# Performance work log

Measured on AMD Instinct MI355X. Metric: run time of the kernel, lower is better.

## Reference

```python
import jax, jax.numpy as jnp
import numpy as np

D_MODEL = 1024
NUM_HEADS = 16
HEAD_DIM = D_MODEL // NUM_HEADS


def setup_inputs() -> dict:
    key = jax.random.key(0)
    ks = jax.random.split(key, 10)
    B, SQ, SKV = 4, 2048, 2048
    s = 1.0 / np.sqrt(D_MODEL)
    return {
        "query": jax.random.normal(ks[0], (B, SQ, D_MODEL), jnp.float32),
        "key_value": jax.random.normal(ks[1], (B, SKV, D_MODEL), jnp.float32),
        "Wq": jax.random.normal(ks[2], (D_MODEL, D_MODEL), jnp.float32) * s,
        "bq": jnp.zeros((D_MODEL,), jnp.float32),
        "Wk": jax.random.normal(ks[3], (D_MODEL, D_MODEL), jnp.float32) * s,
        "bk": jnp.zeros((D_MODEL,), jnp.float32),
        "Wv": jax.random.normal(ks[4], (D_MODEL, D_MODEL), jnp.float32) * s,
        "bv": jnp.zeros((D_MODEL,), jnp.float32),
        "Wo": jax.random.normal(ks[5], (D_MODEL, D_MODEL), jnp.float32) * s,
        "bo": jnp.zeros((D_MODEL,), jnp.float32),
    }


def reference(query, key_value, Wq, bq, Wk, bk, Wv, bv, Wo, bo):
    B, SQ, _ = query.shape
    SKV = key_value.shape[1]
    H, Dh = NUM_HEADS, HEAD_DIM
    # projections (torch Linear: x @ W.T + b); split heads -> (B, H, S, Dh)
    Q = (query @ Wq.T + bq).reshape(B, SQ, H, Dh).transpose(0, 2, 1, 3)
    K = (key_value @ Wk.T + bk).reshape(B, SKV, H, Dh).transpose(0, 2, 1, 3)
    V = (key_value @ Wv.T + bv).reshape(B, SKV, H, Dh).transpose(0, 2, 1, 3)
    scale = jnp.asarray(np.sqrt(Dh), query.dtype)
    scores = jnp.einsum("bhqd,bhkd->bhqk", Q, K) / scale
    weights = jax.nn.softmax(scores, axis=-1)  # dropout is identity in eval
    attn = jnp.einsum("bhqk,bhkd->bhqd", weights, V)
    attn = attn.transpose(0, 2, 1, 3).reshape(B, SQ, H * Dh)
    return attn @ Wo.T + bo
```

## Files before the change

### kernel.cpp

```cpp
#include <hip/hip_runtime.h>

#define NH 16
#define DH 64
#define DM 1024
#define SEQ 2048
#define BATCH 4
#define NT 16

typedef short s16x8 __attribute__((ext_vector_type(8)));
typedef float f32x4 __attribute__((ext_vector_type(4)));

__device__ __forceinline__ unsigned short f2bf(float f) {
  union { float f; unsigned int u; } v; v.f = f;
  unsigned int u = v.u;
  unsigned int r = (u + 0x7fffu + ((u >> 16) & 1u)) >> 16;
  return (unsigned short)r;
}

__device__ __forceinline__ unsigned int pkbf(float a, float b) {
#if __has_builtin(__builtin_amdgcn_cvt_pk_bf16_f32)
  typedef short v2s __attribute__((ext_vector_type(2)));
  v2s r = __builtin_amdgcn_cvt_pk_bf16_f32(a, b);
  union { v2s v; unsigned int u; } cv; cv.v = r;
  return cv.u;
#else
  return (unsigned int)f2bf(a) | ((unsigned int)f2bf(b) << 16);
#endif
}

__device__ __forceinline__ float fexp2(float x) {
#if __has_builtin(__builtin_amdgcn_exp2f)
  return __builtin_amdgcn_exp2f(x);
#else
  return exp2f(x);
#endif
}

__device__ __forceinline__ void gload_lds16(const void* g, void* l) {
  __builtin_amdgcn_global_load_lds(
      (const __attribute__((address_space(1))) unsigned int*)g,
      (__attribute__((address_space(3))) unsigned int*)l, 16, 0, 0);
}

#define GBAR() asm volatile("s_barrier" ::: "memory")

__global__ void convert_all(const float* __restrict__ q, const float* __restrict__ kv,
                            const float* __restrict__ w0, const float* __restrict__ w1,
                            const float* __restrict__ w2, const float* __restrict__ w3,
                            unsigned short* __restrict__ oq, unsigned short* __restrict__ okv,
                            unsigned short* __restrict__ ow0, unsigned short* __restrict__ ow1,
                            unsigned short* __restrict__ ow2, unsigned short* __restrict__ ow3) {
  const int NQ4 = (BATCH * SEQ * DM) / 4;
  const int NW4 = (DM * DM) / 4;
  const int total = NQ4 * 2 + NW4 * 4;
  for (int i = blockIdx.x * blockDim.x + threadIdx.x; i < total;
       i += gridDim.x * blockDim.x) {
    const float* s; unsigned short* d; int off;
    if (i < NQ4)            { s = q;  d = oq;  off = i; }
    else if (i < 2 * NQ4)   { s = kv; d = okv; off = i - NQ4; }
    else {
      int j = i - 2 * NQ4; int wsel = j / NW4; off = j - wsel * NW4;
      s = (wsel == 0) ? w0 : (wsel == 1) ? w1 : (wsel == 2) ? w2 : w3;
      d = (wsel == 0) ? ow0 : (wsel == 1) ? ow1 : (wsel == 2) ? ow2 : ow3;
    }
    float4 v = *(const float4*)(s + (size_t)off * 4);
    ushort4 o;
    o.x = f2bf(v.x); o.y = f2bf(v.y); o.z = f2bf(v.z); o.w = f2bf(v.w);
    *(ushort4*)(d + (size_t)off * 4) = o;
  }
}

template <int NJ>
__device__ __forceinline__ void stage_rows(const unsigned short* __restrict__ src,
                                           int row0, int kt,
                                           unsigned short* __restrict__ dst, int tid) {
  const int sr = tid >> 3;
  const int g8 = ((tid & 7) ^ (sr & 7)) * 8;
  const int wv = tid >> 6;
#pragma unroll
  for (int j = 0; j < NJ; ++j)
    gload_lds16(src + (size_t)(row0 + j * 64 + sr) * DM + kt + g8,
                dst + (j * 8 + wv) * 512);
}

__device__ __forceinline__ void gemm256_tile(const unsigned short* __restrict__ X,
                                             const unsigned short* __restrict__ Wt,
                                             unsigned short* __restrict__ SM,
                                             int m0, int n0, f32x4 (*acc)[4]) {
  const int tid = threadIdx.x;
  const int wv = tid >> 6, lane = tid & 63;
  const int quad = lane >> 4, c = lane & 15;
  const int wr = wv >> 2, wc = wv & 3;
  unsigned short* A0 = SM;
  unsigned short* B0 = SM + 8192;
  unsigned short* A1 = SM + 24576;
  unsigned short* B1 = SM + 24576 + 8192;

  stage_rows<2>(X, m0, 0, A0, tid);
  stage_rows<4>(Wt, n0, 0, B0, tid);
  stage_rows<2>(X, m0, 64, A1, tid);
  stage_rows<4>(Wt, n0, 64, B1, tid);
  asm volatile("s_waitcnt vmcnt(6)" ::: "memory");
  GBAR();

  const int rA0 = wr * 64 + c;
  const int rB0 = wc * 64 + c;
  const int c7 = c & 7;

  for (int t = 0; t < NT; ++t) {
    unsigned short* A_ = (t & 1) ? A1 : A0;
    unsigned short* B_ = (t & 1) ? B1 : B0;
    unsigned short* An = (t & 1) ? A0 : A1;

    s16x8 af[2][2], bf[4][2];
#pragma unroll
    for (int fm = 0; fm < 2; ++fm)
#pragma unroll
      for (int k2 = 0; k2 < 2; ++k2)
        af[fm][k2] = *(const s16x8*)(A_ + (rA0 + fm * 16) * 64 +
                                     (((k2 * 4 + quad) ^ c7) * 8));
#pragma unroll
    for (int fn = 0; fn < 4; ++fn)
#pragma unroll
      for (int k2 = 0; k2 < 2; ++k2)
        bf[fn][k2] = *(const s16x8*)(B_ + (rB0 + fn * 16) * 64 +
                                     (((k2 * 4 + quad) ^ c7) * 8));
    if (t >= 1 && t + 1 < NT)
      stage_rows<2>(X, m0, (t + 1) * 64, An, tid);
    GBAR();
    __builtin_amdgcn_s_setprio(1);
#pragma unroll
    for (int k2 = 0; k2 < 2; ++k2)
#pragma unroll
      for (int fm = 0; fm < 2; ++fm)
#pragma unroll
        for (int fn = 0; fn < 4; ++fn)
          acc[fm][fn] = __builtin_amdgcn_mfma_f32_16x16x32_bf16(
              af[fm][k2], bf[fn][k2], acc[fm][fn], 0, 0, 0);
    __builtin_amdgcn_s_setprio(0);
    GBAR();

#pragma unroll
    for (int fm = 0; fm < 2; ++fm)
#pragma unroll
      for (int k2 = 0; k2 < 2; ++k2)
        af[fm][k2] = *(const s16x8*)(A_ + (rA0 + (fm + 2) * 16) * 64 +
                                     (((k2 * 4 + quad) ^ c7) * 8));
    if (t + 2 < NT) {
      stage_rows<4>(Wt, n0, (t + 2) * 64, B_, tid);
      asm volatile("s_waitcnt vmcnt(4)" ::: "memory");
    } else {
      asm volatile("s_waitcnt vmcnt(0)" ::: "memory");
    }
    GBAR();
    __builtin_amdgcn_s_setprio(1);
#pragma unroll
    for (int k2 = 0; k2 < 2; ++k2)
#pragma unroll
      for (int fm = 0; fm < 2; ++fm)
#pragma unroll
        for (int fn = 0; fn < 4; ++fn)
          acc[fm + 2][fn] = __builtin_amdgcn_mfma_f32_16x16x32_bf16(
              af[fm][k2], bf[fn][k2], acc[fm + 2][fn], 0, 0, 0);
    __builtin_amdgcn_s_setprio(0);
    GBAR();
  }
}

__global__ __launch_bounds__(512, 2)
void gemm_qkv256(const unsigned short* __restrict__ Xq,
                 const unsigned short* __restrict__ Xkv,
                 const unsigned short* __restrict__ W0,
                 const unsigned short* __restrict__ W1,
                 const unsigned short* __restrict__ W2,
                 const float* __restrict__ b0, const float* __restrict__ b1,
                 const float* __restrict__ b2,
                 unsigned short* __restrict__ OQ, unsigned short* __restrict__ OK_,
                 unsigned short* __restrict__ OV) {
  __shared__ alignas(16) unsigned short SM[49152];
  const int m0 = blockIdx.x * 128;
  const int ysel = blockIdx.y >> 2;
  const int n0 = (blockIdx.y & 3) * 256;
  const unsigned short* X = (ysel == 0) ? Xq : Xkv;
  const unsigned short* Wt = (ysel == 0) ? W0 : (ysel == 1) ? W1 : W2;
  const float* bias = (ysel == 0) ? b0 : (ysel == 1) ? b1 : b2;
  unsigned short* Out = (ysel == 0) ? OQ : (ysel == 1) ? OK_ : OV;
  const float scale = (ysel == 0) ? 0.1803368801f : 1.0f;

  f32x4 acc[4][4] = {};
  gemm256_tile(X, Wt, SM, m0, n0, acc);

  const int tid = threadIdx.x;
  const int wv = tid >> 6, lane = tid & 63;
  const int quad = lane >> 4, c = lane & 15;
  const int wr = wv >> 2, wc = wv & 3;
  const int m0w = m0 + wr * 64;
  const int n0w = n0 + wc * 64;
#pragma unroll
  for (int fm = 0; fm < 4; ++fm) {
#pragma unroll
    for (int fn = 0; fn < 4; ++fn) {
      int n = n0w + fn * 16 + c;
      float bv = bias[n];
      int m_base = m0w + fm * 16 + quad * 4;
      if (ysel == 2) {
        int b_ = m_base >> 11, s_ = m_base & 2047, h_ = n >> 6, dh = n & 63;
        size_t idx = (((size_t)(b_ * NH + h_)) * DH + dh) * SEQ + s_;
        ushort4 o4;
        o4.x = f2bf(acc[fm][fn][0] + bv);
        o4.y = f2bf(acc[fm][fn][1] + bv);
        o4.z = f2bf(acc[fm][fn][2] + bv);
        o4.w = f2bf(acc[fm][fn][3] + bv);
        *(ushort4*)(&Out[idx]) = o4;
      } else {
#pragma unroll
        for (int p = 0; p < 4; ++p) {
          int m = m_base + p;
          float val = (acc[fm][fn][p] + bv) * scale;
          int b_ = m >> 11, s_ = m & 2047, h_ = n >> 6, dh = n & 63;
          size_t idx = (((size_t)(b_ * NH + h_)) * SEQ + s_) * DH + dh;
          Out[idx] = f2bf(val);
        }
      }
    }
  }
}

__global__ __launch_bounds__(512, 2)
void gemm_o256(const unsigned short* __restrict__ X,
               const unsigned short* __restrict__ Wt,
               const float* __restrict__ bias, float* __restrict__ Out) {
  __shared__ alignas(16) unsigned short SM[49152];
  const int m0 = blockIdx.x * 128;
  const int n0 = blockIdx.y * 256;
  f32x4 acc[4][4] = {};
  gemm256_tile(X, Wt, SM, m0, n0, acc);

  const int tid = threadIdx.x;
  const int wv = tid >> 6, lane = tid & 63;
  const int quad = lane >> 4, c = lane & 15;
  const int wr = wv >> 2, wc = wv & 3;
  const int m0w = m0 + wr * 64;
  const int n0w = n0 + wc * 64;
#pragma unroll
  for (int fm = 0; fm < 4; ++fm) {
#pragma unroll
    for (int fn = 0; fn < 4; ++fn) {
      int n = n0w + fn * 16 + c;
      float bv = bias[n];
#pragma unroll
      for (int p = 0; p < 4; ++p) {
        int m = m0w + fm * 16 + quad * 4 + p;
        Out[(size_t)m * DM + n] = acc[fm][fn][p] + bv;
      }
    }
  }
}

__global__ __launch_bounds__(256, 4)
void attn_kernel(const unsigned short* __restrict__ Qb,
                 const unsigned short* __restrict__ Kb,
                 const unsigned short* __restrict__ VTb,
                 unsigned short* __restrict__ Ob) {
  __shared__ alignas(16) unsigned short SM[16384];

  const int tid = threadIdx.x, wv_ = tid >> 6, lane = tid & 63;
  const int quad = lane >> 4, c = lane & 15;
  const int bh = blockIdx.x, qb = blockIdx.y;
  const unsigned short* Qp = Qb + (size_t)bh * SEQ * DH;
  const unsigned short* Kp = Kb + (size_t)bh * SEQ * DH;
  const unsigned short* Vp = VTb + (size_t)bh * DH * SEQ;
  const int wq0 = qb * 128 + wv_ * 32;

  s16x8 aq[2][2];
#pragma unroll
  for (int t = 0; t < 2; ++t)
#pragma unroll
    for (int k2 = 0; k2 < 2; ++k2)
      aq[t][k2] = *(const s16x8*)(Qp + (size_t)(wq0 + t * 16 + c) * DH +
                                  k2 * 32 + quad * 8);

  f32x4 ot[4][2] = {};
  float lsum[2] = {};

  const int srow = lane >> 3;
  const int schunk = (lane & 7) ^ srow;

#pragma unroll
  for (int i = 0; i < 2; ++i) {
    int reg = wv_ * 2 + i;
    gload_lds16(Kp + (size_t)(reg * 8 + srow) * DH + schunk * 8,
                (void*)(SM + reg * 512));
    gload_lds16(Vp + (size_t)(reg * 8 + srow) * SEQ + schunk * 8,
                (void*)(SM + 8192 + reg * 512));
  }

  for (int kt = 0; kt < SEQ; kt += 64) {
    const int cur = (kt >> 6) & 1;
    __syncthreads();
    if (kt + 64 < SEQ) {
      const int nxt = cur ^ 1;
#pragma unroll
      for (int i = 0; i < 2; ++i) {
        int reg = wv_ * 2 + i;
        gload_lds16(Kp + (size_t)(kt + 64 + reg * 8 + srow) * DH + schunk * 8,
                    (void*)(SM + nxt * 4096 + reg * 512));
        gload_lds16(Vp + (size_t)(reg * 8 + srow) * SEQ + kt + 64 + schunk * 8,
                    (void*)(SM + 8192 + nxt * 4096 + reg * 512));
      }
    }
    const unsigned short* K_ = SM + cur * 4096;
    const unsigned short* V_ = SM + 8192 + cur * 4096;

    f32x4 s[2][2][2] = {};
#pragma unroll
    for (int k2 = 0; k2 < 2; ++k2) {
      s16x8 ak[2][2];
#pragma unroll
      for (int jp = 0; jp < 2; ++jp)
#pragma unroll
        for (int h = 0; h < 2; ++h) {
          int r = jp * 32 + ((c >> 2) << 3) + h * 4 + (c & 3);
          int g = k2 * 4 + quad;
          ak[jp][h] = *(const s16x8*)(K_ + r * 64 + ((g ^ (r & 7)) * 8));
        }
#pragma unroll
      for (int t = 0; t < 2; ++t)
#pragma unroll
        for (int jp = 0; jp < 2; ++jp)
#pragma unroll
          for (int h = 0; h < 2; ++h)
            s[t][jp][h] = __builtin_amdgcn_mfma_f32_16x16x32_bf16(
                ak[jp][h], aq[t][k2], s[t][jp][h], 0, 0, 0);
    }

    s16x8 bp[2][2];
#pragma unroll
    for (int t = 0; t < 2; ++t)
#pragma unroll
      for (int jp = 0; jp < 2; ++jp) {
        float e00 = fexp2(s[t][jp][0][0]);
        float e01 = fexp2(s[t][jp][0][1]);
        float e02 = fexp2(s[t][jp][0][2]);
        float e03 = fexp2(s[t][jp][0][3]);
        float e10 = fexp2(s[t][jp][1][0]);
        float e11 = fexp2(s[t][jp][1][1]);
        float e12 = fexp2(s[t][jp][1][2]);
        float e13 = fexp2(s[t][jp][1][3]);
        lsum[t] += ((e00 + e01) + (e02 + e03)) + ((e10 + e11) + (e12 + e13));
        union { s16x8 v; unsigned int u[4]; } pk;
        pk.u[0] = pkbf(e00, e01);
        pk.u[1] = pkbf(e02, e03);
        pk.u[2] = pkbf(e10, e11);
        pk.u[3] = pkbf(e12, e13);
        bp[t][jp] = pk.v;
      }

#pragma unroll
    for (int jp = 0; jp < 2; ++jp)
#pragma unroll
      for (int dt = 0; dt < 4; ++dt) {
        int g = jp * 4 + quad;
        int r = dt * 16 + c;
        s16x8 av = *(const s16x8*)(V_ + r * 64 + ((g ^ (r & 7)) * 8));
#pragma unroll
        for (int t = 0; t < 2; ++t)
          ot[dt][t] = __builtin_amdgcn_mfma_f32_16x16x32_bf16(
              av, bp[t][jp], ot[dt][t], 0, 0, 0);
      }
  }

#pragma unroll
  for (int t = 0; t < 2; ++t) {
    lsum[t] += __shfl_xor(lsum[t], 16);
    lsum[t] += __shfl_xor(lsum[t], 32);
  }

  __syncthreads();

  unsigned short* Lq = SM + wv_ * (32 * 72);
#pragma unroll
  for (int t = 0; t < 2; ++t) {
    float inv = 1.0f / lsum[t];
#pragma unroll
    for (int dt = 0; dt < 4; ++dt) {
      unsigned int w01 = pkbf(ot[dt][t][0] * inv, ot[dt][t][1] * inv);
      unsigned int w23 = pkbf(ot[dt][t][2] * inv, ot[dt][t][3] * inv);
      unsigned short* p = Lq + (t * 16 + c) * 72 + dt * 16 + quad * 4;
      *(unsigned int*)(p) = w01;
      *(unsigned int*)(p + 2) = w23;
    }
  }
  const int b_ = bh >> 4, h_ = bh & 15;
  const int ql = lane >> 1, hf = lane & 1;
  const unsigned short* Lr = Lq + ql * 72 + hf * 32;
  unsigned short* Og = Ob + ((size_t)(b_ * SEQ + wq0 + ql)) * DM + h_ * 64 + hf * 32;
#pragma unroll
  for (int j = 0; j < 4; ++j) {
    s16x8 v = *(const s16x8*)(Lr + j * 8);
    *(s16x8*)(Og + j * 8) = v;
  }
}

extern "C" void kernel_launch(void* const* d_in, const int* in_sizes, int n_in,
                              void* d_out, int out_size, void* d_ws, size_t ws_size,
                              hipStream_t stream) {
  const float* q  = (const float*)d_in[0];
  const float* kv = (const float*)d_in[1];
  const float* Wq = (const float*)d_in[2];
  const float* bq = (const float*)d_in[3];
  const float* Wk = (const float*)d_in[4];
  const float* bk = (const float*)d_in[5];
  const float* Wv = (const float*)d_in[6];
  const float* bv = (const float*)d_in[7];
  const float* Wo = (const float*)d_in[8];
  const float* bo = (const float*)d_in[9];

  char* ws = (char*)d_ws;
  const size_t MB = 1024 * 1024;
  unsigned short* q_bf  = (unsigned short*)(ws);
  unsigned short* kv_bf = (unsigned short*)(ws + 16 * MB);
  unsigned short* wq_bf = (unsigned short*)(ws + 32 * MB);
  unsigned short* wk_bf = (unsigned short*)(ws + 34 * MB);
  unsigned short* wv_bf = (unsigned short*)(ws + 36 * MB);
  unsigned short* wo_bf = (unsigned short*)(ws + 38 * MB);
  unsigned short* Qb    = (unsigned short*)(ws + 40 * MB);
  unsigned short* Kb    = (unsigned short*)(ws + 56 * MB);
  unsigned short* VTb   = (unsigned short*)(ws + 72 * MB);
  unsigned short* attn  = (unsigned short*)(ws + 88 * MB);

  convert_all<<<2048, 256, 0, stream>>>(q, kv, Wq, Wk, Wv, Wo,
                                        q_bf, kv_bf, wq_bf, wk_bf, wv_bf, wo_bf);
  gemm_qkv256<<<dim3(64, 12), 512, 0, stream>>>(q_bf, kv_bf, wq_bf, wk_bf, wv_bf,
                                                bq, bk, bv, Qb, Kb, VTb);
  attn_kernel<<<dim3(64, 16), 256, 0, stream>>>(Qb, Kb, VTb, attn);
  gemm_o256<<<dim3(64, 4), 512, 0, stream>>>(attn, wo_bf, bo, (float*)d_out);
}
```

Baseline: 328.3 us.

## Enlarge projection GEMM tiles to 256x256 with 8-phase pipeline and block swizzle

Replaces the 128x256 GEMM tile with a 256x256 tile in both projection GEMMs. Each wave now computes 128x64 with 32 accumulators, and the K loop becomes an eight-phase schedule that interleaves half-slab global-to-LDS loads with LDS reads and MFMA bursts. Workgroup indices are swizzled so neighbouring blocks share operand rows. The aim is more reuse per loaded byte and better L2 locality, at the cost of 128KB LDS, more registers and only 384/128 blocks, which may underfill the CUs.

```diff
diff --git a/kernel.cpp b/kernel.cpp
--- a/kernel.cpp
+++ b/kernel.cpp
@@ -43,6 +43,7 @@
 }
 
 #define GBAR() asm volatile("s_barrier" ::: "memory")
+#define LG0()  asm volatile("s_waitcnt lgkmcnt(0)" ::: "memory")
 
 __global__ void convert_all(const float* __restrict__ q, const float* __restrict__ kv,
                             const float* __restrict__ w0, const float* __restrict__ w1,
@@ -70,134 +71,163 @@
   }
 }
 
-template <int NJ>
-__device__ __forceinline__ void stage_rows(const unsigned short* __restrict__ src,
+__device__ __forceinline__ void stage_slab(const unsigned short* __restrict__ src,
                                            int row0, int kt,
-                                           unsigned short* __restrict__ dst, int tid) {
+                                           unsigned short* __restrict__ lds, int tid) {
   const int sr = tid >> 3;
   const int g8 = ((tid & 7) ^ (sr & 7)) * 8;
-  const int wv = tid >> 6;
-#pragma unroll
-  for (int j = 0; j < NJ; ++j)
-    gload_lds16(src + (size_t)(row0 + j * 64 + sr) * DM + kt + g8,
-                dst + (j * 8 + wv) * 512);
-}
-
-__device__ __forceinline__ void gemm256_tile(const unsigned short* __restrict__ X,
-                                             const unsigned short* __restrict__ Wt,
-                                             unsigned short* __restrict__ SM,
-                                             int m0, int n0, f32x4 (*acc)[4]) {
+  gload_lds16(src + (size_t)(row0 + sr) * DM + kt + g8,
+              lds + (tid >> 6) * 512);
+}
+
+__device__ __forceinline__ void rd4(const unsigned short* __restrict__ base,
+                                    int xg, s16x8 (&f)[4]) {
+#pragma unroll
+  for (int j = 0; j < 4; ++j)
+    f[j] = *(const s16x8*)(base + j * 1024 + xg);
+}
+
+template <int H>
+__device__ __forceinline__ void mm16(s16x8 (&af)[4], s16x8 (&bf)[4],
+                                     f32x4 (*acc)[4]) {
+  __builtin_amdgcn_s_setprio(1);
+#pragma unroll
+  for (int j = 0; j < 4; ++j)
+#pragma unroll
+    for (int fn = 0; fn < 4; ++fn)
+      acc[H * 4 + j][fn] = __builtin_amdgcn_mfma_f32_16x16x32_bf16(
+          af[j], bf[fn], acc[H * 4 + j][fn], 0, 0, 0);
+  __builtin_amdgcn_s_setprio(0);
+}
+
+__device__ __forceinline__ void gemm8p_tile(const unsigned short* __restrict__ X,
+                                            const unsigned short* __restrict__ Wt,
+                                            unsigned short* __restrict__ SM,
+                                            int m0, int n0, f32x4 (*acc)[4]) {
   const int tid = threadIdx.x;
   const int wv = tid >> 6, lane = tid & 63;
   const int quad = lane >> 4, c = lane & 15;
   const int wr = wv >> 2, wc = wv & 3;
-  unsigned short* A0 = SM;
-  unsigned short* B0 = SM + 8192;
-  unsigned short* A1 = SM + 24576;
-  unsigned short* B1 = SM + 24576 + 8192;
-
-  stage_rows<2>(X, m0, 0, A0, tid);
-  stage_rows<4>(Wt, n0, 0, B0, tid);
-  stage_rows<2>(X, m0, 64, A1, tid);
-  stage_rows<4>(Wt, n0, 64, B1, tid);
-  asm volatile("s_waitcnt vmcnt(6)" ::: "memory");
+  const int rA = (wr * 128 + c) * 64;
+  const int rB = (wc * 64 + c) * 64;
+  const int xg0 = (quad ^ (c & 7)) * 8;
+  const int xg1 = ((4 + quad) ^ (c & 7)) * 8;
+  const int A0 = 0, B0 = 16384, A1 = 32768, B1 = 49152;
+
+  s16x8 af[4], bf[4];
+
+  stage_slab(Wt, n0,       0, SM + B0,         tid);
+  stage_slab(Wt, n0 + 64,  0, SM + B0 + 4096,  tid);
+  stage_slab(Wt, n0 + 128, 0, SM + B0 + 8192,  tid);
+  stage_slab(Wt, n0 + 192, 0, SM + B0 + 12288, tid);
+  stage_slab(X,  m0,       0, SM + A0,         tid);
+  stage_slab(X,  m0 + 128, 0, SM + A0 + 8192,  tid);
+  stage_slab(X,  m0 + 64,  0, SM + A0 + 4096,  tid);
+  stage_slab(X,  m0 + 192, 0, SM + A0 + 12288, tid);
+  stage_slab(Wt, n0,       64, SM + B1,        tid);
+  stage_slab(Wt, n0 + 64,  64, SM + B1 + 4096, tid);
+  stage_slab(X,  m0,       64, SM + A1,        tid);
+  stage_slab(X,  m0 + 128, 64, SM + A1 + 8192, tid);
+  asm volatile("s_waitcnt vmcnt(4)" ::: "memory");
   GBAR();
 
-  const int rA0 = wr * 64 + c;
-  const int rB0 = wc * 64 + c;
-  const int c7 = c & 7;
-
-  for (int t = 0; t < NT; ++t) {
-    unsigned short* A_ = (t & 1) ? A1 : A0;
-    unsigned short* B_ = (t & 1) ? B1 : B0;
-    unsigned short* An = (t & 1) ? A0 : A1;
-
-    s16x8 af[2][2], bf[4][2];
-#pragma unroll
-    for (int fm = 0; fm < 2; ++fm)
-#pragma unroll
-      for (int k2 = 0; k2 < 2; ++k2)
-        af[fm][k2] = *(const s16x8*)(A_ + (rA0 + fm * 16) * 64 +
-                                     (((k2 * 4 + quad) ^ c7) * 8));
-#pragma unroll
-    for (int fn = 0; fn < 4; ++fn)
-#pragma unroll
-      for (int k2 = 0; k2 < 2; ++k2)
-        bf[fn][k2] = *(const s16x8*)(B_ + (rB0 + fn * 16) * 64 +
-                                     (((k2 * 4 + quad) ^ c7) * 8));
-    if (t >= 1 && t + 1 < NT)
-      stage_rows<2>(X, m0, (t + 1) * 64, An, tid);
-    GBAR();
-    __builtin_amdgcn_s_setprio(1);
-#pragma unroll
-    for (int k2 = 0; k2 < 2; ++k2)
-#pragma unroll
-      for (int fm = 0; fm < 2; ++fm)
-#pragma unroll
-        for (int fn = 0; fn < 4; ++fn)
-          acc[fm][fn] = __builtin_amdgcn_mfma_f32_16x16x32_bf16(
-              af[fm][k2], bf[fn][k2], acc[fm][fn], 0, 0, 0);
-    __builtin_amdgcn_s_setprio(0);
-    GBAR();
-
-#pragma unroll
-    for (int fm = 0; fm < 2; ++fm)
-#pragma unroll
-      for (int k2 = 0; k2 < 2; ++k2)
-        af[fm][k2] = *(const s16x8*)(A_ + (rA0 + (fm + 2) * 16) * 64 +
-                                     (((k2 * 4 + quad) ^ c7) * 8));
-    if (t + 2 < NT) {
-      stage_rows<4>(Wt, n0, (t + 2) * 64, B_, tid);
+  for (int i = 0; i < NT / 2; ++i) {
+    const int t1k = (2 * i + 1) * 64;
+    const int t2 = 2 * i + 2, t3 = 2 * i + 3;
+    const int t2k = t2 * 64, t3k = t3 * 64;
+
+    rd4(SM + B0 + rB, xg0, bf);
+    rd4(SM + A0 + rA, xg0, af);
+    stage_slab(Wt, n0 + 128, t1k, SM + B1 + 8192,  tid);
+    stage_slab(Wt, n0 + 192, t1k, SM + B1 + 12288, tid);
+    stage_slab(X,  m0 + 64,  t1k, SM + A1 + 4096,  tid);
+    stage_slab(X,  m0 + 192, t1k, SM + A1 + 12288, tid);
+    GBAR(); LG0(); mm16<0>(af, bf, acc); GBAR();
+
+    rd4(SM + A0 + rA + 4096, xg0, af);
+    GBAR(); LG0(); mm16<1>(af, bf, acc); GBAR();
+
+    rd4(SM + B0 + rB, xg1, bf);
+    rd4(SM + A0 + rA, xg1, af);
+    GBAR(); LG0(); mm16<0>(af, bf, acc); GBAR();
+
+    rd4(SM + A0 + rA + 4096, xg1, af);
+    if (t2 < NT) {
+      stage_slab(Wt, n0,       t2k, SM + B0,        tid);
+      stage_slab(Wt, n0 + 64,  t2k, SM + B0 + 4096, tid);
+      stage_slab(X,  m0,       t2k, SM + A0,        tid);
+      stage_slab(X,  m0 + 128, t2k, SM + A0 + 8192, tid);
       asm volatile("s_waitcnt vmcnt(4)" ::: "memory");
     } else {
       asm volatile("s_waitcnt vmcnt(0)" ::: "memory");
     }
-    GBAR();
-    __builtin_amdgcn_s_setprio(1);
-#pragma unroll
-    for (int k2 = 0; k2 < 2; ++k2)
-#pragma unroll
-      for (int fm = 0; fm < 2; ++fm)
-#pragma unroll
-        for (int fn = 0; fn < 4; ++fn)
-          acc[fm + 2][fn] = __builtin_amdgcn_mfma_f32_16x16x32_bf16(
-              af[fm][k2], bf[fn][k2], acc[fm + 2][fn], 0, 0, 0);
-    __builtin_amdgcn_s_setprio(0);
-    GBAR();
+    GBAR(); LG0(); mm16<1>(af, bf, acc); GBAR();
+
+    rd4(SM + B1 + rB, xg0, bf);
+    rd4(SM + A1 + rA, xg0, af);
+    if (t2 < NT) {
+      stage_slab(Wt, n0 + 128, t2k, SM + B0 + 8192,  tid);
+      stage_slab(Wt, n0 + 192, t2k, SM + B0 + 12288, tid);
+      stage_slab(X,  m0 + 64,  t2k, SM + A0 + 4096,  tid);
+      stage_slab(X,  m0 + 192, t2k, SM + A0 + 12288, tid);
+    }
+    GBAR(); LG0(); mm16<0>(af, bf, acc); GBAR();
+
+    rd4(SM + A1 + rA + 4096, xg0, af);
+    GBAR(); LG0(); mm16<1>(af, bf, acc); GBAR();
+
+    rd4(SM + B1 + rB, xg1, bf);
+    rd4(SM + A1 + rA, xg1, af);
+    GBAR(); LG0(); mm16<0>(af, bf, acc); GBAR();
+
+    rd4(SM + A1 + rA + 4096, xg1, af);
+    if (t3 < NT) {
+      stage_slab(Wt, n0,       t3k, SM + B1,        tid);
+      stage_slab(Wt, n0 + 64,  t3k, SM + B1 + 4096, tid);
+      stage_slab(X,  m0,       t3k, SM + A1,        tid);
+      stage_slab(X,  m0 + 128, t3k, SM + A1 + 8192, tid);
+      asm volatile("s_waitcnt vmcnt(4)" ::: "memory");
+    } else {
+      asm volatile("s_waitcnt vmcnt(0)" ::: "memory");
+    }
+    GBAR(); LG0(); mm16<1>(af, bf, acc); GBAR();
   }
 }
 
 __global__ __launch_bounds__(512, 2)
-void gemm_qkv256(const unsigned short* __restrict__ Xq,
-                 const unsigned short* __restrict__ Xkv,
-                 const unsigned short* __restrict__ W0,
-                 const unsigned short* __restrict__ W1,
-                 const unsigned short* __restrict__ W2,
-                 const float* __restrict__ b0, const float* __restrict__ b1,
-                 const float* __restrict__ b2,
-                 unsigned short* __restrict__ OQ, unsigned short* __restrict__ OK_,
-                 unsigned short* __restrict__ OV) {
-  __shared__ alignas(16) unsigned short SM[49152];
-  const int m0 = blockIdx.x * 128;
-  const int ysel = blockIdx.y >> 2;
-  const int n0 = (blockIdx.y & 3) * 256;
+void gemm_qkv8p(const unsigned short* __restrict__ Xq,
+                const unsigned short* __restrict__ Xkv,
+                const unsigned short* __restrict__ W0,
+                const unsigned short* __restrict__ W1,
+                const unsigned short* __restrict__ W2,
+                const float* __restrict__ b0, const float* __restrict__ b1,
+                const float* __restrict__ b2,
+                unsigned short* __restrict__ OQ, unsigned short* __restrict__ OK_,
+                unsigned short* __restrict__ OV) {
+  __shared__ alignas(16) unsigned short SM[65536];
+  const int wg = blockIdx.y * 32 + blockIdx.x;
+  const int swz = (wg & 7) * 48 + (wg >> 3);
+  const int m0 = (swz & 31) * 256;
+  const int yy = swz >> 5;
+  const int ysel = yy >> 2;
+  const int n0 = (yy & 3) * 256;
   const unsigned short* X = (ysel == 0) ? Xq : Xkv;
   const unsigned short* Wt = (ysel == 0) ? W0 : (ysel == 1) ? W1 : W2;
   const float* bias = (ysel == 0) ? b0 : (ysel == 1) ? b1 : b2;
   unsigned short* Out = (ysel == 0) ? OQ : (ysel == 1) ? OK_ : OV;
   const float scale = (ysel == 0) ? 0.1803368801f : 1.0f;
 
-  f32x4 acc[4][4] = {};
-  gemm256_tile(X, Wt, SM, m0, n0, acc);
+  f32x4 acc[8][4] = {};
+  gemm8p_tile(X, Wt, SM, m0, n0, acc);
 
   const int tid = threadIdx.x;
   const int wv = tid >> 6, lane = tid & 63;
   const int quad = lane >> 4, c = lane & 15;
   const int wr = wv >> 2, wc = wv & 3;
-  const int m0w = m0 + wr * 64;
+  const int m0w = m0 + wr * 128;
   const int n0w = n0 + wc * 64;
 #pragma unroll
-  for (int fm = 0; fm < 4; ++fm) {
+  for (int fm = 0; fm < 8; ++fm) {
 #pragma unroll
     for (int fn = 0; fn < 4; ++fn) {
       int n = n0w + fn * 16 + c;
@@ -227,23 +257,25 @@
 }
 
 __global__ __launch_bounds__(512, 2)
-void gemm_o256(const unsigned short* __restrict__ X,
-               const unsigned short* __restrict__ Wt,
-               const float* __restrict__ bias, float* __restrict__ Out) {
-  __shared__ alignas(16) unsigned short SM[49152];
-  const int m0 = blockIdx.x * 128;
-  const int n0 = blockIdx.y * 256;
-  f32x4 acc[4][4] = {};
-  gemm256_tile(X, Wt, SM, m0, n0, acc);
+void gemm_o8p(const unsigned short* __restrict__ X,
+              const unsigned short* __restrict__ Wt,
+              const float* __restrict__ bias, float* __restrict__ Out) {
+  __shared__ alignas(16) unsigned short SM[65536];
+  const int wg = blockIdx.y * 32 + blockIdx.x;
+  const int swz = (wg & 7) * 16 + (wg >> 3);
+  const int m0 = (swz & 31) * 256;
+  const int n0 = (swz >> 5) * 256;
+  f32x4 acc[8][4] = {};
+  gemm8p_tile(X, Wt, SM, m0, n0, acc);
 
   const int tid = threadIdx.x;
   const int wv = tid >> 6, lane = tid & 63;
   const int quad = lane >> 4, c = lane & 15;
   const int wr = wv >> 2, wc = wv & 3;
-  const int m0w = m0 + wr * 64;
+  const int m0w = m0 + wr * 128;
   const int n0w = n0 + wc * 64;
 #pragma unroll
-  for (int fm = 0; fm < 4; ++fm) {
+  for (int fm = 0; fm < 8; ++fm) {
 #pragma unroll
     for (int fn = 0; fn < 4; ++fn) {
       int n = n0w + fn * 16 + c;
@@ -431,8 +463,8 @@
 
   convert_all<<<2048, 256, 0, stream>>>(q, kv, Wq, Wk, Wv, Wo,
                                         q_bf, kv_bf, wq_bf, wk_bf, wv_bf, wo_bf);
-  gemm_qkv256<<<dim3(64, 12), 512, 0, stream>>>(q_bf, kv_bf, wq_bf, wk_bf, wv_bf,
-                                                bq, bk, bv, Qb, Kb, VTb);
+  gemm_qkv8p<<<dim3(32, 12), 512, 0, stream>>>(q_bf, kv_bf, wq_bf, wk_bf, wv_bf,
+                                               bq, bk, bv, Qb, Kb, VTb);
   attn_kernel<<<dim3(64, 16), 256, 0, stream>>>(Qb, Kb, VTb, attn);
-  gemm_o256<<<dim3(64, 4), 512, 0, stream>>>(attn, wo_bf, bo, (float*)d_out);
-}
+  gemm_o8p<<<dim3(32, 4), 512, 0, stream>>>(attn, wo_bf, bo, (float*)d_out);
+}
```

New measurement: 339.9 us. 1.04x slower.
